# Performance work log

Measured on AMD Instinct MI355X. Metric: run time of the kernel, lower is better.

The kernel has to match this reference:

```python
import jax, jax.numpy as jnp
import numpy as np
import math

jax.config.update("jax_enable_x64", True)

# cfg constants
N = 4096
DIM = 16
SA = 2.0        # sigma_a
SR = 0.5        # sigma_r
V_SCALE = 1.0
R_H = 6.0
TAU_H = 0.5
K0_KUR = 0.05
TAU_KUR = 2.0
EPS = 1e-7      # acosh clamp epsilon (K=1 curvature)
D_MIN = 0.08    # distance floor in pairwise_dist


def setup_inputs() -> dict:
    key = jax.random.key(0)
    d_star = SA * SR / (SA - SR) * math.log(SA / SR)
    r_init = 0.5 * d_star
    hs = jax.random.normal(key, (N, DIM), dtype=jnp.float64) * r_init
    ht = jnp.sqrt(1.0 + jnp.sum(hs ** 2, axis=-1, keepdims=True))
    h = jnp.concatenate([ht, hs], axis=-1)  # [N, DIM+1] on the hyperboloid
    return {"h": h}


def reference(h):
    """Pairwise hyperbolic distance -> LJ coupling K_geo -> Lorentz-log force F,
    plus LJ potential energy E. Matmul form: no [N,N,dim+1] intermediates."""
    n1 = h.shape[-1]
    metric = jnp.concatenate([-jnp.ones((1,), h.dtype), jnp.ones((n1 - 1,), h.dtype)])
    # Lorentz inner products for all pairs: [N, N] (fp64)
    inn = (h * metric) @ h.T
    # geodesic distance d = acosh(clamp(-<hi,hj>_L, 1+eps))  (K = 1)
    D = jnp.arccosh(jnp.clip(-inn, 1.0 + EPS))
    eye = jnp.eye(N, dtype=h.dtype)
    # exact pairwise_dist semantics: zero diag, add D_MIN to off-diag entries < D_MIN
    D_pair = D * (1.0 - eye) + D_MIN * (((D < D_MIN) & (eye < 0.5)).astype(h.dtype))

    # _build_K in float32 (K_local == 1 since use_dyn_curv=False, learn_K=False)
    D_f = D_pair.astype(jnp.float32)
    eye32 = eye.astype(jnp.float32)
    D_eff = jnp.clip(D_f, 0.05)  # (D / sqrt(clamp(Ki*Kj,1e-4))).clamp(min=0.05) with K_local=1
    dVdd = jnp.exp(-D_eff / SR) / SR - jnp.exp(-D_eff / SA) / SA
    K_geo = -dVdd * V_SCALE * (1.0 - eye32)
    K_geo = K_geo * jax.nn.sigmoid((R_H - D_eff) / TAU_H)  # causal horizon
    K_kur = K0_KUR * jnp.exp(-D_f / TAU_KUR) * (1.0 - eye32)

    # _force: F_i = sum_j K_geo_ij * log_{h_i}(h_j)
    # log_x(y) = d / sqrt(<x,y>^2 - 1) * (y + <x,y> x)
    denom = jnp.sqrt(jnp.clip(inn ** 2 - 1.0, 1e-15))
    C = K_geo.astype(h.dtype) * D / denom  # [N, N]; diag is 0 since K_geo diag is 0
    F = C @ h + jnp.sum(C * inn, axis=-1, keepdims=True) * h  # [N, DIM+1]
    F_norm = jnp.clip(jnp.linalg.norm(F, axis=-1, keepdims=True), 1e-8)
    F = F * jnp.minimum(6.0 / F_norm, 1.0)

    # lj_potential energy on D_pair
    V = V_SCALE * (jnp.exp(-D_pair / SA) - jnp.exp(-D_pair / SR))
    E = jnp.sum(V * (1.0 - eye)) * 0.5
    return F, E
```

## Files before the change

### kernel.cpp

```cpp
#include <hip/hip_runtime.h>

#define NPTS 4096
#define DIMP 17
#define ROWP 20
#define RROW 21
#define JPB  128
#define IPB  128
#define NSLAB (NPTS / JPB)
#define NIB   (NPTS / IPB)
#define EOFF  (NSLAB * NPTS * ROWP)
#define NEP   (NIB * NSLAB)
#define REDF  (384 * RROW)

typedef float v2f __attribute__((ext_vector_type(2)));
typedef float v4f __attribute__((ext_vector_type(4)));

__global__ __launch_bounds__(256, 4) void hydra_pair_kernel(
    const float* __restrict__ h, float* __restrict__ ws,
    float* __restrict__ out, const int use_ws) {
    const int tid   = threadIdx.x;
    const int lane  = tid & 63;
    const int wid   = tid >> 6;
    const int i0    = blockIdx.x * IPB;
    const int i1    = i0 + lane;
    const int i2    = i0 + 64 + lane;
    const int jbase = blockIdx.y * JPB;

    __shared__ __align__(16) float lds[REDF + 16];

    for (int idx = tid; idx < JPB * DIMP; idx += 256) {
        const int j = idx / DIMP;
        const int k = idx - j * DIMP;
        lds[j * ROWP + k] = h[jbase * DIMP + idx];
    }

    float nh1[DIMP], nh2[DIMP];
#pragma unroll
    for (int k = 0; k < DIMP; ++k) nh1[k] = -h[i1 * DIMP + k];
#pragma unroll
    for (int k = 0; k < DIMP; ++k) nh2[k] = -h[i2 * DIMP + k];
    nh1[0] = -nh1[0];
    nh2[0] = -nh2[0];

    __syncthreads();

    float ac1[DIMP], ac2[DIMP];
#pragma unroll
    for (int k = 0; k < DIMP; ++k) { ac1[k] = 0.0f; ac2[k] = 0.0f; }
    float sm1 = 0.0f, sm2 = 0.0f;
    float eacc = 0.0f;

    const float* rowp = lds + (wid * 32) * ROWP;
#pragma unroll 2
    for (int jj = 0; jj < 32; ++jj, rowp += ROWP) {
        const v4f a0 = ((const v4f*)rowp)[0];
        const v4f a1 = ((const v4f*)rowp)[1];
        const v4f a2 = ((const v4f*)rowp)[2];
        const v4f a3 = ((const v4f*)rowp)[3];
        const float a16 = rowp[16];
        const float hj[DIMP] = {a0.x, a0.y, a0.z, a0.w, a1.x, a1.y, a1.z, a1.w,
                                a2.x, a2.y, a2.z, a2.w, a3.x, a3.y, a3.z, a3.w, a16};

        float p0 = nh1[0] * hj[0], p1 = nh1[1] * hj[1];
        float q0 = nh2[0] * hj[0], q1 = nh2[1] * hj[1];
#pragma unroll
        for (int k = 2; k < 16; k += 2) {
            p0 = fmaf(nh1[k], hj[k], p0);     p1 = fmaf(nh1[k + 1], hj[k + 1], p1);
            q0 = fmaf(nh2[k], hj[k], q0);     q1 = fmaf(nh2[k + 1], hj[k + 1], q1);
        }
        const float m1 = fmaf(nh1[16], a16, p0 + p1);
        const float m2 = fmaf(nh2[16], a16, q0 + q1);

        const float x1  = m1 - 1.0f;
        const float ss1 = fmaxf(fmaf(m1, m1, -1.0f), 2e-7f);
        const float r1  = __builtin_amdgcn_rsqf(ss1);
        const float sq1 = ss1 * r1;
        const float w1  = (x1 - sq1) + 1.0f;
        const float d1  = -__logf(w1);
        const float t1  = __builtin_amdgcn_sqrtf(w1);
        const float u1  = w1 * w1;
        const float g1  = u1 * __builtin_amdgcn_rcpf(u1 + 6.1442123533e-6f);
        const float K1  = fmaf(0.5f, t1, -2.0f * u1) * g1;
        const float C1  = K1 * d1 * r1;
        const float x2  = m2 - 1.0f;
        const float ss2 = fmaxf(fmaf(m2, m2, -1.0f), 2e-7f);
        const float r2  = __builtin_amdgcn_rsqf(ss2);
        const float sq2 = ss2 * r2;
        const float w2  = (x2 - sq2) + 1.0f;
        const float d2  = -__logf(w2);
        const float t2  = __builtin_amdgcn_sqrtf(w2);
        const float u2  = w2 * w2;
        const float g2  = u2 * __builtin_amdgcn_rcpf(u2 + 6.1442123533e-6f);
        const float K2  = fmaf(0.5f, t2, -2.0f * u2) * g2;
        const float C2  = K2 * d2 * r2;

        eacc += (t1 - u1) + (t2 - u2);
        sm1 = fmaf(C1, m1, sm1);
        sm2 = fmaf(C2, m2, sm2);
#pragma unroll
        for (int k = 0; k < DIMP; ++k) {
            ac1[k] = fmaf(C1, hj[k], ac1[k]);
            ac2[k] = fmaf(C2, hj[k], ac2[k]);
        }
    }

    ac1[0] = fmaf(-sm1, nh1[0], ac1[0]);
    ac2[0] = fmaf(-sm2, nh2[0], ac2[0]);
#pragma unroll
    for (int k = 1; k < DIMP; ++k) {
        ac1[k] = fmaf(sm1, nh1[k], ac1[k]);
        ac2[k] = fmaf(sm2, nh2[k], ac2[k]);
    }

#pragma unroll
    for (int off = 32; off > 0; off >>= 1) eacc += __shfl_xor(eacc, off);

    __syncthreads();
    if (wid > 0) {
        float* dA = lds + ((wid - 1) * 64 + lane) * RROW;
        float* dB = lds + ((192 + (wid - 1) * 64 + lane)) * RROW;
#pragma unroll
        for (int k = 0; k < DIMP; ++k) { dA[k] = ac1[k]; dB[k] = ac2[k]; }
        if (lane == 0) lds[REDF + wid] = eacc;
    }
    __syncthreads();

    if (wid == 0) {
        const float esum = eacc + lds[REDF + 1] + lds[REDF + 2] + lds[REDF + 3];
#pragma unroll
        for (int q = 0; q < 3; ++q) {
            const float* sA = lds + (q * 64 + lane) * RROW;
            const float* sB = lds + ((192 + q * 64 + lane)) * RROW;
#pragma unroll
            for (int k = 0; k < DIMP; ++k) { ac1[k] += sA[k]; ac2[k] += sB[k]; }
        }
        if (use_ws) {
            float* w1p = ws + ((size_t)blockIdx.y * NPTS + i1) * ROWP;
            float* w2p = ws + ((size_t)blockIdx.y * NPTS + i2) * ROWP;
#pragma unroll
            for (int k = 0; k < DIMP; ++k) { w1p[k] = ac1[k]; w2p[k] = ac2[k]; }
            if (lane == 0) ws[EOFF + blockIdx.y * NIB + blockIdx.x] = esum;
        } else {
#pragma unroll
            for (int k = 0; k < DIMP; ++k) {
                atomicAdd(&out[i1 * DIMP + k], ac1[k]);
                atomicAdd(&out[i2 * DIMP + k], ac2[k]);
            }
            if (lane == 0) atomicAdd(&out[NPTS * DIMP], esum);
        }
    }
}

__global__ __launch_bounds__(256) void hydra_finalize_kernel(
    const float* __restrict__ ws, float* __restrict__ out, const int use_ws) {
    const int tid  = threadIdx.x;
    const int lane = tid & 63;
    const int q    = tid >> 6;
    const int i    = blockIdx.x * 64 + lane;

    __shared__ __align__(16) float red[3 * 64 * RROW + 8];

    float v[DIMP];
#pragma unroll
    for (int k = 0; k < DIMP; ++k) v[k] = 0.0f;

    if (use_ws) {
#pragma unroll
        for (int ssl = 0; ssl < NSLAB / 4; ++ssl) {
            const int s = q * (NSLAB / 4) + ssl;
            const float* row = ws + ((size_t)s * NPTS + i) * ROWP;
            const v4f b0 = ((const v4f*)row)[0];
            const v4f b1 = ((const v4f*)row)[1];
            const v4f b2 = ((const v4f*)row)[2];
            const v4f b3 = ((const v4f*)row)[3];
            v[0]  += b0.x; v[1]  += b0.y; v[2]  += b0.z; v[3]  += b0.w;
            v[4]  += b1.x; v[5]  += b1.y; v[6]  += b1.z; v[7]  += b1.w;
            v[8]  += b2.x; v[9]  += b2.y; v[10] += b2.z; v[11] += b2.w;
            v[12] += b3.x; v[13] += b3.y; v[14] += b3.z; v[15] += b3.w;
            v[16] += row[16];
        }
        if (q > 0) {
            float* dst = red + ((q - 1) * 64 + lane) * RROW;
#pragma unroll
            for (int k = 0; k < DIMP; ++k) dst[k] = v[k];
        }
        __syncthreads();
        if (q == 0) {
#pragma unroll
            for (int qq = 0; qq < 3; ++qq) {
                const float* src = red + (qq * 64 + lane) * RROW;
#pragma unroll
                for (int k = 0; k < DIMP; ++k) v[k] += src[k];
            }
        }
    } else if (q == 0) {
#pragma unroll
        for (int k = 0; k < DIMP; ++k) v[k] = out[i * DIMP + k];
    }

    if (q == 0) {
        float ss = 0.0f;
#pragma unroll
        for (int k = 0; k < DIMP; ++k) ss = fmaf(v[k], v[k], ss);
        const float nrm   = sqrtf(ss);
        const float scale = fminf(6.0f / fmaxf(nrm, 1e-8f), 1.0f);
#pragma unroll
        for (int k = 0; k < DIMP; ++k) out[i * DIMP + k] = v[k] * scale;
    }

    if (blockIdx.x == 0) {
        if (use_ws) {
            float e = 0.0f;
#pragma unroll
            for (int t = 0; t < NEP / 256; ++t) e += ws[EOFF + tid + t * 256];
#pragma unroll
            for (int off = 32; off > 0; off >>= 1) e += __shfl_xor(e, off);
            __shared__ float es[4];
            if (lane == 0) es[q] = e;
            __syncthreads();
            if (tid == 0) out[NPTS * DIMP] = 0.5f * (es[0] + es[1] + es[2] + es[3]);
        } else {
            if (tid == 0) out[NPTS * DIMP] *= 0.5f;
        }
    }
}

extern "C" void kernel_launch(void* const* d_in, const int* in_sizes, int n_in,
                              void* d_out, int out_size, void* d_ws, size_t ws_size,
                              hipStream_t stream) {
    const float* h = (const float*)d_in[0];
    float* out = (float*)d_out;
    float* ws  = (float*)d_ws;

    const size_t need = (size_t)(EOFF + NEP) * sizeof(float);
    const int use_ws = (ws_size >= need) ? 1 : 0;
    if (!use_ws) {
        hipMemsetAsync(d_out, 0, (size_t)out_size * sizeof(float), stream);
    }

    dim3 grid(NIB, NSLAB);
    hydra_pair_kernel<<<grid, 256, 0, stream>>>(h, ws, out, use_ws);
    hydra_finalize_kernel<<<64, 256, 0, stream>>>(ws, out, use_ws);
}
```

Before: 44.18 us.

## Stream j-rows through scalar loads instead of LDS, one i per lane

Drops the LDS staging of the j-slab. Each wave now loads its 32 j rows straight from global memory with inline-asm s_load_dwordx16 into scalar registers, double-buffered and overlapped with the pair math. Each lane now handles one i-point instead of two, which doubles the number of i-blocks and halves the accumulator registers. The cost is less ILP per thread, an explicit lgkmcnt wait each step, and twice as many workspace partial rows for the finalize kernel to read, since NEP doubles.

New measurement: 39.49 us. -10.6%, faster.

```diff
diff --git a/kernel.cpp b/kernel.cpp
--- a/kernel.cpp
+++ b/kernel.cpp
@@ -5,122 +5,112 @@
 #define ROWP 20
 #define RROW 21
 #define JPB  128
-#define IPB  128
 #define NSLAB (NPTS / JPB)
-#define NIB   (NPTS / IPB)
+#define NIB   (NPTS / 64)
 #define EOFF  (NSLAB * NPTS * ROWP)
 #define NEP   (NIB * NSLAB)
-#define REDF  (384 * RROW)
-
-typedef float v2f __attribute__((ext_vector_type(2)));
-typedef float v4f __attribute__((ext_vector_type(4)));
-
-__global__ __launch_bounds__(256, 4) void hydra_pair_kernel(
+#define REDF  (192 * RROW)
+#define MAXOFF 278460u
+
+typedef float v4f  __attribute__((ext_vector_type(4)));
+typedef float v16f __attribute__((ext_vector_type(16)));
+
+#define SWAIT() do {                                        \
+    asm volatile("s_waitcnt lgkmcnt(0)" ::: "memory");      \
+    __builtin_amdgcn_sched_barrier(0);                      \
+} while (0)
+
+#define SLOAD(B, B16, OFF) do {                                         \
+    const char* _p = hb + (OFF);                                        \
+    asm volatile("s_load_dwordx16 %0, %1, 0x0"                          \
+                 : "=&s"(B) : "s"(_p));                                 \
+    asm volatile("s_load_dword %0, %1, 0x40"                            \
+                 : "=&s"(B16) : "s"(_p));                               \
+} while (0)
+
+#define PAIR(B, B16) do {                                               \
+    float p0 = nh[0] * (B)[0], p1 = nh[1] * (B)[1];                     \
+    p0 = fmaf(nh[2],  (B)[2],  p0);  p1 = fmaf(nh[3],  (B)[3],  p1);    \
+    p0 = fmaf(nh[4],  (B)[4],  p0);  p1 = fmaf(nh[5],  (B)[5],  p1);    \
+    p0 = fmaf(nh[6],  (B)[6],  p0);  p1 = fmaf(nh[7],  (B)[7],  p1);    \
+    p0 = fmaf(nh[8],  (B)[8],  p0);  p1 = fmaf(nh[9],  (B)[9],  p1);    \
+    p0 = fmaf(nh[10], (B)[10], p0);  p1 = fmaf(nh[11], (B)[11], p1);    \
+    p0 = fmaf(nh[12], (B)[12], p0);  p1 = fmaf(nh[13], (B)[13], p1);    \
+    p0 = fmaf(nh[14], (B)[14], p0);  p1 = fmaf(nh[15], (B)[15], p1);    \
+    const float m  = fmaf(nh[16], (B16), p0 + p1);         \
+    const float ss = fmaxf(fmaf(m, m, -1.0f), 2e-7f);       \
+    const float r  = __builtin_amdgcn_rsqf(ss);             \
+    const float sq = ss * r;                                  \
+    const float w  = ((m - 1.0f) - sq) + 1.0f;              \
+    const float d  = -__logf(w);                                        \
+    const float t  = __builtin_amdgcn_sqrtf(w);           \
+    const float u  = w * w;                                \
+    const float sg = u * __builtin_amdgcn_rcpf(u + 6.1442123533e-6f);   \
+    const float K  = fmaf(0.5f, t, -2.0f * u) * sg;                     \
+    const float C  = K * d * r;                                         \
+    eacc += (t - u);                                                    \
+    sm = fmaf(C, m, sm);                                                \
+    ac[0]  = fmaf(C, (B)[0],  ac[0]);  ac[1]  = fmaf(C, (B)[1],  ac[1]);\
+    ac[2]  = fmaf(C, (B)[2],  ac[2]);  ac[3]  = fmaf(C, (B)[3],  ac[3]);\
+    ac[4]  = fmaf(C, (B)[4],  ac[4]);  ac[5]  = fmaf(C, (B)[5],  ac[5]);\
+    ac[6]  = fmaf(C, (B)[6],  ac[6]);  ac[7]  = fmaf(C, (B)[7],  ac[7]);\
+    ac[8]  = fmaf(C, (B)[8],  ac[8]);  ac[9]  = fmaf(C, (B)[9],  ac[9]);\
+    ac[10] = fmaf(C, (B)[10], ac[10]); ac[11] = fmaf(C, (B)[11], ac[11]);\
+    ac[12] = fmaf(C, (B)[12], ac[12]); ac[13] = fmaf(C, (B)[13], ac[13]);\
+    ac[14] = fmaf(C, (B)[14], ac[14]); ac[15] = fmaf(C, (B)[15], ac[15]);\
+    ac[16] = fmaf(C, (B16), ac[16]);                                    \
+} while (0)
+
+__global__ __launch_bounds__(256) void hydra_pair_kernel(
     const float* __restrict__ h, float* __restrict__ ws,
     float* __restrict__ out, const int use_ws) {
-    const int tid   = threadIdx.x;
-    const int lane  = tid & 63;
-    const int wid   = tid >> 6;
-    const int i0    = blockIdx.x * IPB;
-    const int i1    = i0 + lane;
-    const int i2    = i0 + 64 + lane;
-    const int jbase = blockIdx.y * JPB;
-
-    __shared__ __align__(16) float lds[REDF + 16];
-
-    for (int idx = tid; idx < JPB * DIMP; idx += 256) {
-        const int j = idx / DIMP;
-        const int k = idx - j * DIMP;
-        lds[j * ROWP + k] = h[jbase * DIMP + idx];
-    }
-
-    float nh1[DIMP], nh2[DIMP];
-#pragma unroll
-    for (int k = 0; k < DIMP; ++k) nh1[k] = -h[i1 * DIMP + k];
-#pragma unroll
-    for (int k = 0; k < DIMP; ++k) nh2[k] = -h[i2 * DIMP + k];
-    nh1[0] = -nh1[0];
-    nh2[0] = -nh2[0];
-
-    __syncthreads();
-
-    float ac1[DIMP], ac2[DIMP];
-#pragma unroll
-    for (int k = 0; k < DIMP; ++k) { ac1[k] = 0.0f; ac2[k] = 0.0f; }
-    float sm1 = 0.0f, sm2 = 0.0f;
-    float eacc = 0.0f;
-
-    const float* rowp = lds + (wid * 32) * ROWP;
-#pragma unroll 2
-    for (int jj = 0; jj < 32; ++jj, rowp += ROWP) {
-        const v4f a0 = ((const v4f*)rowp)[0];
-        const v4f a1 = ((const v4f*)rowp)[1];
-        const v4f a2 = ((const v4f*)rowp)[2];
-        const v4f a3 = ((const v4f*)rowp)[3];
-        const float a16 = rowp[16];
-        const float hj[DIMP] = {a0.x, a0.y, a0.z, a0.w, a1.x, a1.y, a1.z, a1.w,
-                                a2.x, a2.y, a2.z, a2.w, a3.x, a3.y, a3.z, a3.w, a16};
-
-        float p0 = nh1[0] * hj[0], p1 = nh1[1] * hj[1];
-        float q0 = nh2[0] * hj[0], q1 = nh2[1] * hj[1];
-#pragma unroll
-        for (int k = 2; k < 16; k += 2) {
-            p0 = fmaf(nh1[k], hj[k], p0);     p1 = fmaf(nh1[k + 1], hj[k + 1], p1);
-            q0 = fmaf(nh2[k], hj[k], q0);     q1 = fmaf(nh2[k + 1], hj[k + 1], q1);
-        }
-        const float m1 = fmaf(nh1[16], a16, p0 + p1);
-        const float m2 = fmaf(nh2[16], a16, q0 + q1);
-
-        const float x1  = m1 - 1.0f;
-        const float ss1 = fmaxf(fmaf(m1, m1, -1.0f), 2e-7f);
-        const float r1  = __builtin_amdgcn_rsqf(ss1);
-        const float sq1 = ss1 * r1;
-        const float w1  = (x1 - sq1) + 1.0f;
-        const float d1  = -__logf(w1);
-        const float t1  = __builtin_amdgcn_sqrtf(w1);
-        const float u1  = w1 * w1;
-        const float g1  = u1 * __builtin_amdgcn_rcpf(u1 + 6.1442123533e-6f);
-        const float K1  = fmaf(0.5f, t1, -2.0f * u1) * g1;
-        const float C1  = K1 * d1 * r1;
-        const float x2  = m2 - 1.0f;
-        const float ss2 = fmaxf(fmaf(m2, m2, -1.0f), 2e-7f);
-        const float r2  = __builtin_amdgcn_rsqf(ss2);
-        const float sq2 = ss2 * r2;
-        const float w2  = (x2 - sq2) + 1.0f;
-        const float d2  = -__logf(w2);
-        const float t2  = __builtin_amdgcn_sqrtf(w2);
-        const float u2  = w2 * w2;
-        const float g2  = u2 * __builtin_amdgcn_rcpf(u2 + 6.1442123533e-6f);
-        const float K2  = fmaf(0.5f, t2, -2.0f * u2) * g2;
-        const float C2  = K2 * d2 * r2;
-
-        eacc += (t1 - u1) + (t2 - u2);
-        sm1 = fmaf(C1, m1, sm1);
-        sm2 = fmaf(C2, m2, sm2);
-#pragma unroll
-        for (int k = 0; k < DIMP; ++k) {
-            ac1[k] = fmaf(C1, hj[k], ac1[k]);
-            ac2[k] = fmaf(C2, hj[k], ac2[k]);
-        }
-    }
-
-    ac1[0] = fmaf(-sm1, nh1[0], ac1[0]);
-    ac2[0] = fmaf(-sm2, nh2[0], ac2[0]);
-#pragma unroll
-    for (int k = 1; k < DIMP; ++k) {
-        ac1[k] = fmaf(sm1, nh1[k], ac1[k]);
-        ac2[k] = fmaf(sm2, nh2[k], ac2[k]);
-    }
+    const int tid  = threadIdx.x;
+    const int lane = tid & 63;
+    const int wid  = tid >> 6;
+    const int i    = blockIdx.x * 64 + lane;
+
+    __shared__ float lds[REDF + 16];
+
+    float nh[DIMP];
+#pragma unroll
+    for (int k = 0; k < DIMP; ++k) nh[k] = -h[i * DIMP + k];
+    nh[0] = -nh[0];
+
+    float ac[DIMP];
+#pragma unroll
+    for (int k = 0; k < DIMP; ++k) ac[k] = 0.0f;
+    float sm = 0.0f, eacc = 0.0f;
+
+    const char* hb = (const char*)h;
+    const unsigned base_off = (unsigned)__builtin_amdgcn_readfirstlane(
+        (int)((blockIdx.y * JPB + wid * 32) * (DIMP * 4)));
+
+    v16f bA, bB; float tA, tB;
+    SLOAD(bA, tA, base_off);
+    for (int jj = 0; jj < 32; jj += 2) {
+        unsigned o1 = base_off + (unsigned)(jj + 1) * 68u;
+        unsigned o2 = base_off + (unsigned)(jj + 2) * 68u;
+        if (o2 > MAXOFF) o2 = MAXOFF;
+        SWAIT();
+        SLOAD(bB, tB, o1);
+        PAIR(bA, tA);
+        SWAIT();
+        SLOAD(bA, tA, o2);
+        PAIR(bB, tB);
+    }
+
+    ac[0] = fmaf(-sm, nh[0], ac[0]);
+#pragma unroll
+    for (int k = 1; k < DIMP; ++k) ac[k] = fmaf(sm, nh[k], ac[k]);
 
 #pragma unroll
     for (int off = 32; off > 0; off >>= 1) eacc += __shfl_xor(eacc, off);
 
     __syncthreads();
     if (wid > 0) {
-        float* dA = lds + ((wid - 1) * 64 + lane) * RROW;
-        float* dB = lds + ((192 + (wid - 1) * 64 + lane)) * RROW;
-#pragma unroll
-        for (int k = 0; k < DIMP; ++k) { dA[k] = ac1[k]; dB[k] = ac2[k]; }
+        float* dst = lds + ((wid - 1) * 64 + lane) * RROW;
+#pragma unroll
+        for (int k = 0; k < DIMP; ++k) dst[k] = ac[k];
         if (lane == 0) lds[REDF + wid] = eacc;
     }
     __syncthreads();
@@ -129,23 +119,18 @@
         const float esum = eacc + lds[REDF + 1] + lds[REDF + 2] + lds[REDF + 3];
 #pragma unroll
         for (int q = 0; q < 3; ++q) {
-            const float* sA = lds + (q * 64 + lane) * RROW;
-            const float* sB = lds + ((192 + q * 64 + lane)) * RROW;
-#pragma unroll
-            for (int k = 0; k < DIMP; ++k) { ac1[k] += sA[k]; ac2[k] += sB[k]; }
+            const float* src = lds + (q * 64 + lane) * RROW;
+#pragma unroll
+            for (int k = 0; k < DIMP; ++k) ac[k] += src[k];
         }
         if (use_ws) {
-            float* w1p = ws + ((size_t)blockIdx.y * NPTS + i1) * ROWP;
-            float* w2p = ws + ((size_t)blockIdx.y * NPTS + i2) * ROWP;
-#pragma unroll
-            for (int k = 0; k < DIMP; ++k) { w1p[k] = ac1[k]; w2p[k] = ac2[k]; }
+            float* dst = ws + ((size_t)blockIdx.y * NPTS + i) * ROWP;
+#pragma unroll
+            for (int k = 0; k < DIMP; ++k) dst[k] = ac[k];
             if (lane == 0) ws[EOFF + blockIdx.y * NIB + blockIdx.x] = esum;
         } else {
 #pragma unroll
-            for (int k = 0; k < DIMP; ++k) {
-                atomicAdd(&out[i1 * DIMP + k], ac1[k]);
-                atomicAdd(&out[i2 * DIMP + k], ac2[k]);
-            }
+            for (int k = 0; k < DIMP; ++k) atomicAdd(&out[i * DIMP + k], ac[k]);
             if (lane == 0) atomicAdd(&out[NPTS * DIMP], esum);
         }
     }
```
